# Kernel optimization log

Hardware: AMD Instinct MI355X
Metric: run time of the kernel (lower is better)

Reference implementation:

```python
import jax, jax.numpy as jnp
import numpy as np

B, N, E = 4, 10000, 640000
IN, HID, OUT, H = 128, 64, 64, 2


def _lin(key, fi, fo):
    kw, kb = jax.random.split(key)
    w = jax.random.normal(kw, (fi, fo), dtype=jnp.float32) / np.sqrt(fi)
    b = jnp.zeros((fo,), dtype=jnp.float32)
    return w, b


def setup_inputs() -> dict:
    key = jax.random.key(0)
    ks = jax.random.split(key, 12)
    x = jax.random.normal(ks[0], (B, N, IN), dtype=jnp.float32)
    edge_index = jax.random.randint(ks[1], (2, E), 0, B * N, dtype=jnp.int64)
    # layer 1: TransformerConv(IN -> HID, heads=H, concat=False)
    Wq1, bq1 = _lin(ks[2], IN, H * HID)
    Wk1, bk1 = _lin(ks[3], IN, H * HID)
    Wv1, bv1 = _lin(ks[4], IN, H * HID)
    Ws1, bs1 = _lin(ks[5], IN, HID)  # root/skip (concat=False -> out_channels)
    # layer 2: TransformerConv(HID -> OUT, heads=H, concat=False), no activation
    Wq2, bq2 = _lin(ks[6], HID, H * OUT)
    Wk2, bk2 = _lin(ks[7], HID, H * OUT)
    Wv2, bv2 = _lin(ks[8], HID, H * OUT)
    Ws2, bs2 = _lin(ks[9], HID, OUT)
    return dict(x=x, edge_index=edge_index,
                Wq1=Wq1, bq1=bq1, Wk1=Wk1, bk1=bk1, Wv1=Wv1, bv1=bv1, Ws1=Ws1, bs1=bs1,
                Wq2=Wq2, bq2=bq2, Wk2=Wk2, bk2=bk2, Wv2=Wv2, bv2=bv2, Ws2=Ws2, bs2=bs2)


def transformer_conv(x, src, dst, Wq, bq, Wk, bk, Wv, bv, Ws, bs, heads, ch):
    """PyG TransformerConv with concat=False (mean over heads) + root skip."""
    Nn = x.shape[0]
    q = (x @ Wq + bq).reshape(Nn, heads, ch)
    k = (x @ Wk + bk).reshape(Nn, heads, ch)
    v = (x @ Wv + bv).reshape(Nn, heads, ch)
    scale = 1.0 / np.sqrt(ch)
    # edge-wise attention logits: q_i . k_j / sqrt(ch)   [E, H]
    alpha = jnp.einsum('ehc,ehc->eh', q[dst], k[src]) * scale
    # numerically stable softmax over incoming edges of each destination node
    m = jax.ops.segment_max(alpha, dst, num_segments=Nn)  # [Nn, H]
    e = jnp.exp(alpha - m[dst])
    denom = jax.ops.segment_sum(e, dst, num_segments=Nn)  # [Nn, H]
    msg = jax.ops.segment_sum(e[:, :, None] * v[src], dst, num_segments=Nn)  # [Nn,H,C]
    out = msg / jnp.maximum(denom, 1e-16)[:, :, None]
    out = out.mean(axis=1)  # concat=False -> average heads
    return out + x @ Ws + bs  # root_weight skip


def reference(x, edge_index,
              Wq1, bq1, Wk1, bk1, Wv1, bv1, Ws1, bs1,
              Wq2, bq2, Wk2, bk2, Wv2, bv2, Ws2, bs2):
    bsz, n, _ = x.shape
    xf = x.reshape(bsz * n, IN)
    src, dst = edge_index[0], edge_index[1]
    h = transformer_conv(xf, src, dst, Wq1, bq1, Wk1, bk1, Wv1, bv1, Ws1, bs1, H, HID)
    h = jax.nn.leaky_relu(h, 0.1)
    o = transformer_conv(h, src, dst, Wq2, bq2, Wk2, bk2, Wv2, bv2, Ws2, bs2, H, OUT)
    return o.reshape(bsz, n, OUT)
```

## Files before the change

### kernel.cpp

```cpp
#include <hip/hip_runtime.h>
#include <math.h>

#define NN    40000
#define HEADS 2
#define CHN   64
#define NC    448
#define QSC   192

#define SCAN_BLK 256
#define NBLK ((NN + SCAN_BLK - 1) / SCAN_BLK)

__device__ __forceinline__ unsigned short f2bf(float f) {
  unsigned int u = __float_as_uint(f);
  unsigned int r = u + 0x7fffu + ((u >> 16) & 1u);
  return (unsigned short)(r >> 16);
}

__global__ void detect_k(const int* __restrict__ w, int* __restrict__ flag) {
  int lane = threadIdx.x & 63;
  int v = 0;
#pragma unroll
  for (int i = 0; i < 4; ++i) v |= w[2 * (lane + 64 * i) + 1];
#pragma unroll
  for (int o = 32; o; o >>= 1) v |= __shfl_xor(v, o);
  if (lane == 0 && blockIdx.x == 0) *flag = (v == 0) ? 1 : 0;
}

__global__ void decode_k(const int* __restrict__ w, const int* __restrict__ flag,
                         int* __restrict__ srcs, int* __restrict__ dsts,
                         int* __restrict__ deg, int E) {
  int e = blockIdx.x * blockDim.x + threadIdx.x;
  if (e >= E) return;
  int s, d;
  if (*flag) { s = w[2 * e]; d = w[2 * (E + e)]; }
  else       { s = w[e];     d = w[E + e]; }
  srcs[e] = s;
  dsts[e] = d;
  atomicAdd(&deg[d], 1);
}

__global__ void pack_all(const float* __restrict__ Wq1, const float* __restrict__ bq1,
                         const float* __restrict__ Wk1, const float* __restrict__ bk1,
                         const float* __restrict__ Wv1, const float* __restrict__ bv1,
                         const float* __restrict__ Ws1, const float* __restrict__ bs1,
                         const float* __restrict__ Wq2, const float* __restrict__ bq2,
                         const float* __restrict__ Wk2, const float* __restrict__ bk2,
                         const float* __restrict__ Wv2, const float* __restrict__ bv2,
                         const float* __restrict__ Ws2, const float* __restrict__ bs2,
                         float* __restrict__ B1, float* __restrict__ bias1,
                         float* __restrict__ B2, float* __restrict__ bias2) {
  int i = blockIdx.x * blockDim.x + threadIdx.x;
  if (i < 57344) {
    int k = i / NC, c = i % NC;
    float v;
    if (c < 128)      v = Wq1[k * 128 + c];
    else if (c < 256) v = Wk1[k * 128 + (c - 128)];
    else if (c < 384) v = Wv1[k * 128 + (c - 256)];
    else              v = Ws1[k * 64 + (c - 384)];
    B1[i] = v;
  } else if (i < 86016) {
    int j = i - 57344;
    int k = j / NC, c = j % NC;
    float v;
    if (c < 128)      v = Wq2[k * 128 + c];
    else if (c < 256) v = Wk2[k * 128 + (c - 128)];
    else if (c < 384) v = Wv2[k * 128 + (c - 256)];
    else              v = Ws2[k * 64 + (c - 384)];
    B2[j] = v;
  } else if (i < 86464) {
    int c = i - 86016;
    float v;
    if (c < 128)      v = bq1[c];
    else if (c < 256) v = bk1[c - 128];
    else if (c < 384) v = bv1[c - 256];
    else              v = bs1[c - 384];
    bias1[c] = v;
  } else if (i < 86912) {
    int c = i - 86464;
    float v;
    if (c < 128)      v = bq2[c];
    else if (c < 256) v = bk2[c - 128];
    else if (c < 384) v = bv2[c - 256];
    else              v = bs2[c - 384];
    bias2[c] = v;
  }
}

__global__ __launch_bounds__(SCAN_BLK) void bsum_k(const int* __restrict__ deg,
                                                   int* __restrict__ bsum) {
  int t = threadIdx.x;
  int i = blockIdx.x * SCAN_BLK + t;
  int v = (i < NN) ? deg[i] : 0;
#pragma unroll
  for (int o = 32; o; o >>= 1) v += __shfl_xor(v, o);
  __shared__ int ws[4];
  if ((t & 63) == 0) ws[t >> 6] = v;
  __syncthreads();
  if (t == 0) bsum[blockIdx.x] = ws[0] + ws[1] + ws[2] + ws[3];
}

__global__ __launch_bounds__(SCAN_BLK) void bscan_k(const int* __restrict__ bsum,
                                                    int* __restrict__ boff) {
  int t = threadIdx.x;
  int lane = t & 63, w = t >> 6;
  int v = (t < NBLK) ? bsum[t] : 0;
  int incl = v;
#pragma unroll
  for (int o = 1; o < 64; o <<= 1) {
    int u = __shfl_up(incl, o);
    if (lane >= o) incl += u;
  }
  __shared__ int wsum[4];
  if (lane == 63) wsum[w] = incl;
  __syncthreads();
  int woff = 0;
  for (int j = 0; j < w; ++j) woff += wsum[j];
  if (t < NBLK) boff[t] = woff + incl - v;
}

__global__ __launch_bounds__(SCAN_BLK) void rpwrite_k(const int* __restrict__ deg,
    const int* __restrict__ boff, int* __restrict__ rp, int* __restrict__ cur) {
  int t = threadIdx.x;
  int i = blockIdx.x * SCAN_BLK + t;
  int v = (i < NN) ? deg[i] : 0;
  int lane = t & 63, w = t >> 6;
  int incl = v;
#pragma unroll
  for (int o = 1; o < 64; o <<= 1) {
    int u = __shfl_up(incl, o);
    if (lane >= o) incl += u;
  }
  __shared__ int wsum[4];
  if (lane == 63) wsum[w] = incl;
  __syncthreads();
  int woff = 0;
  for (int j = 0; j < w; ++j) woff += wsum[j];
  int ex = boff[blockIdx.x] + woff + incl - v;
  if (i < NN) { rp[i] = ex; cur[i] = ex; }
  if (i == NN - 1) rp[NN] = ex + v;
}

__global__ void scatter_k(const int* __restrict__ srcs, const int* __restrict__ dsts,
                          int* __restrict__ cur, int* __restrict__ col, int E) {
  int e = blockIdx.x * blockDim.x + threadIdx.x;
  if (e < E) {
    int p = atomicAdd(&cur[dsts[e]], 1);
    col[p] = srcs[e];
  }
}

__global__ __launch_bounds__(256) void gemm_bias(const float* __restrict__ A,
    const float* __restrict__ Bm, const float* __restrict__ bias,
    float* __restrict__ QS, unsigned short* __restrict__ KVH, int M, int K) {
  __shared__ __align__(16) float As[32][68];
  __shared__ __align__(16) float Bs[32][64];
  int bm = blockIdx.y << 6, bn = blockIdx.x << 6;
  int tid = threadIdx.x;
  int tr = (tid >> 4) << 2;
  int tc = (tid & 15) << 2;
  float acc[4][4] = {};
  for (int k0 = 0; k0 < K; k0 += 32) {
#pragma unroll
    for (int t = 0; t < 2; ++t) {
      int i = tid + (t << 8);
      int m = i >> 3, k4 = (i & 7) << 2;
      const float4 va = *(const float4*)(A + (size_t)(bm + m) * K + k0 + k4);
      As[k4 + 0][m] = va.x; As[k4 + 1][m] = va.y;
      As[k4 + 2][m] = va.z; As[k4 + 3][m] = va.w;
      int kb = i >> 4, n4 = (i & 15) << 2;
      *(float4*)&Bs[kb][n4] = *(const float4*)(Bm + (size_t)(k0 + kb) * NC + bn + n4);
    }
    __syncthreads();
#pragma unroll
    for (int kk = 0; kk < 32; ++kk) {
      const float4 av = *(const float4*)&As[kk][tr];
      const float4 bv = *(const float4*)&Bs[kk][tc];
      float a[4] = {av.x, av.y, av.z, av.w};
      float b[4] = {bv.x, bv.y, bv.z, bv.w};
#pragma unroll
      for (int i2 = 0; i2 < 4; ++i2)
#pragma unroll
        for (int j = 0; j < 4; ++j) acc[i2][j] += a[i2] * b[j];
    }
    __syncthreads();
  }
  const int c0 = bn + tc;
  const float4 bb = *(const float4*)&bias[c0];
#pragma unroll
  for (int i2 = 0; i2 < 4; ++i2) {
    int row = bm + tr + i2;
    float4 o;
    o.x = acc[i2][0] + bb.x; o.y = acc[i2][1] + bb.y;
    o.z = acc[i2][2] + bb.z; o.w = acc[i2][3] + bb.w;
    if (c0 < 128) {
      *(float4*)(QS + (size_t)row * QSC + c0) = o;
    } else if (c0 < 384) {
      int isV = (c0 >= 256);
      int kc = c0 - 128 - (isV << 7);
      int hh = kc >> 6, ch = kc & 63;
      size_t off = (size_t)row * 256 + hh * 128 + (ch >> 2) * 8 + (isV << 2);
      ushort4 w4;
      w4.x = f2bf(o.x); w4.y = f2bf(o.y); w4.z = f2bf(o.z); w4.w = f2bf(o.w);
      *(ushort4*)(KVH + off) = w4;
    } else {
      *(float4*)(QS + (size_t)row * QSC + 128 + (c0 - 384)) = o;
    }
  }
}

__global__ __launch_bounds__(128) void agg_fused(const float* __restrict__ QS,
    const unsigned short* __restrict__ KVH,
    const int* __restrict__ rp, const int* __restrict__ col,
    float* __restrict__ out, int act) {
  int dst = blockIdx.x;
  int h = threadIdx.x >> 6;
  int lane = threadIdx.x & 63;
  int g = lane >> 4;
  int sl = lane & 15;
  const float scale = 0.125f;

  float4 q4 = *(const float4*)(QS + (size_t)dst * QSC + h * 64 + 4 * sl);
  q4.x *= scale; q4.y *= scale; q4.z *= scale; q4.w *= scale;
  const unsigned short* __restrict__ kvb = KVH + h * 128 + sl * 8;

  float m = -INFINITY, d = 0.f;
  float4 acc = {0.f, 0.f, 0.f, 0.f};
  int e0 = rp[dst], e1 = rp[dst + 1];

  int e = e0 + g;
  if (e < e1) {
    int sCur = col[e];
    int en = e + 4;
    int sNxt = (en < e1) ? col[en] : sCur;
    uint4 uC = *(const uint4*)(kvb + (size_t)sCur * 256);
    while (true) {
      uint4 uN = *(const uint4*)(kvb + (size_t)sNxt * 256);
      int enn = e + 8;
      int sNN = (enn < e1) ? col[enn] : sNxt;
      float k0 = __uint_as_float(uC.x << 16);
      float k1 = __uint_as_float(uC.x & 0xffff0000u);
      float k2 = __uint_as_float(uC.y << 16);
      float k3 = __uint_as_float(uC.y & 0xffff0000u);
      float p = q4.x * k0 + q4.y * k1 + q4.z * k2 + q4.w * k3;
      p += __shfl_xor(p, 1); p += __shfl_xor(p, 2);
      p += __shfl_xor(p, 4); p += __shfl_xor(p, 8);
      float mn = fmaxf(m, p);
      float corr = __expf(m - mn);
      float w = __expf(p - mn);
      float v0 = __uint_as_float(uC.z << 16);
      float v1 = __uint_as_float(uC.z & 0xffff0000u);
      float v2 = __uint_as_float(uC.w << 16);
      float v3 = __uint_as_float(uC.w & 0xffff0000u);
      d = d * corr + w;
      acc.x = acc.x * corr + w * v0;
      acc.y = acc.y * corr + w * v1;
      acc.z = acc.z * corr + w * v2;
      acc.w = acc.w * corr + w * v3;
      m = mn;
      e += 4;
      if (e >= e1) break;
      uC = uN; sNxt = sNN;
    }
  }

#pragma unroll
  for (int o = 16; o <= 32; o <<= 1) {
    float m2 = __shfl_xor(m, o);
    float d2 = __shfl_xor(d, o);
    float ax = __shfl_xor(acc.x, o), ay = __shfl_xor(acc.y, o);
    float az = __shfl_xor(acc.z, o), aw = __shfl_xor(acc.w, o);
    float mn = fmaxf(m, m2);
    float c1 = __expf(fmaxf(m - mn, -88.f));
    float c2 = __expf(fmaxf(m2 - mn, -88.f));
    d = d * c1 + d2 * c2;
    acc.x = acc.x * c1 + ax * c2;
    acc.y = acc.y * c1 + ay * c2;
    acc.z = acc.z * c1 + az * c2;
    acc.w = acc.w * c1 + aw * c2;
    m = mn;
  }
  float inv = 1.0f / fmaxf(d, 1e-16f);
  float4 r = {acc.x * inv, acc.y * inv, acc.z * inv, acc.w * inv};

  __shared__ float s1[64];
  if (h == 1 && g == 0) *(float4*)&s1[4 * sl] = r;
  __syncthreads();
  if (h == 0 && g == 0) {
    const float4 rr = *(const float4*)&s1[4 * sl];
    const float4 sk = *(const float4*)(QS + (size_t)dst * QSC + 128 + 4 * sl);
    float4 o;
    o.x = 0.5f * (r.x + rr.x) + sk.x;
    o.y = 0.5f * (r.y + rr.y) + sk.y;
    o.z = 0.5f * (r.z + rr.z) + sk.z;
    o.w = 0.5f * (r.w + rr.w) + sk.w;
    if (act) {
      o.x = o.x > 0.f ? o.x : 0.1f * o.x;
      o.y = o.y > 0.f ? o.y : 0.1f * o.y;
      o.z = o.z > 0.f ? o.z : 0.1f * o.z;
      o.w = o.w > 0.f ? o.w : 0.1f * o.w;
    }
    *(float4*)(out + (size_t)dst * CHN + 4 * sl) = o;
  }
}

extern "C" void kernel_launch(void* const* d_in, const int* in_sizes, int n_in,
                              void* d_out, int out_size, void* d_ws, size_t ws_size,
                              hipStream_t stream) {
  const float* x = (const float*)d_in[0];
  const int* ei_raw = (const int*)d_in[1];
  const float *Wq1 = (const float*)d_in[2],  *bq1 = (const float*)d_in[3],
              *Wk1 = (const float*)d_in[4],  *bk1 = (const float*)d_in[5],
              *Wv1 = (const float*)d_in[6],  *bv1 = (const float*)d_in[7],
              *Ws1 = (const float*)d_in[8],  *bs1 = (const float*)d_in[9],
              *Wq2 = (const float*)d_in[10], *bq2 = (const float*)d_in[11],
              *Wk2 = (const float*)d_in[12], *bk2 = (const float*)d_in[13],
              *Wv2 = (const float*)d_in[14], *bv2 = (const float*)d_in[15],
              *Ws2 = (const float*)d_in[16], *bs2 = (const float*)d_in[17];
  float* out = (float*)d_out;
  const int E = in_sizes[1] / 2;

  char* base = (char*)d_ws;
  size_t off = 0;
  auto take = [&](size_t bytes) {
    char* p = base + off;
    off += (bytes + 255) & ~(size_t)255;
    return p;
  };
  float* B1    = (float*)take((size_t)128 * NC * 4);
  float* bias1 = (float*)take(NC * 4);
  float* B2    = (float*)take((size_t)64 * NC * 4);
  float* bias2 = (float*)take(NC * 4);
  int*   flag  = (int*)take(256);
  int*   deg   = (int*)take((size_t)NN * 4);
  int*   rp    = (int*)take((size_t)(NN + 1) * 4);
  int*   cur   = (int*)take((size_t)(NN + 1) * 4);
  int*   bsum  = (int*)take((size_t)NBLK * 4);
  int*   boff  = (int*)take((size_t)NBLK * 4);
  int*   srcs  = (int*)take((size_t)E * 4);
  int*   dsts  = (int*)take((size_t)E * 4);
  int*   col   = (int*)take((size_t)E * 4);
  float* QS    = (float*)take((size_t)NN * QSC * 4);
  unsigned short* KVH = (unsigned short*)take((size_t)NN * 256 * 2);
  float* Hbuf  = (float*)take((size_t)NN * CHN * 4);
  (void)ws_size; (void)n_in; (void)out_size;

  hipMemsetAsync(deg, 0, (size_t)NN * 4, stream);
  pack_all<<<(86912 + 255) / 256, 256, 0, stream>>>(
      Wq1, bq1, Wk1, bk1, Wv1, bv1, Ws1, bs1,
      Wq2, bq2, Wk2, bk2, Wv2, bv2, Ws2, bs2, B1, bias1, B2, bias2);
  detect_k<<<1, 64, 0, stream>>>(ei_raw, flag);
  decode_k<<<(E + 255) / 256, 256, 0, stream>>>(ei_raw, flag, srcs, dsts, deg, E);
  bsum_k<<<NBLK, SCAN_BLK, 0, stream>>>(deg, bsum);
  bscan_k<<<1, SCAN_BLK, 0, stream>>>(bsum, boff);
  rpwrite_k<<<NBLK, SCAN_BLK, 0, stream>>>(deg, boff, rp, cur);
  scatter_k<<<(E + 255) / 256, 256, 0, stream>>>(srcs, dsts, cur, col, E);

  gemm_bias<<<dim3(NC / 64, NN / 64), 256, 0, stream>>>(x, B1, bias1, QS, KVH, NN, 128);
  agg_fused<<<NN, 128, 0, stream>>>(QS, KVH, rp, col, Hbuf, 1);

  gemm_bias<<<dim3(NC / 64, NN / 64), 256, 0, stream>>>(Hbuf, B2, bias2, QS, KVH, NN, 64);
  agg_fused<<<NN, 128, 0, stream>>>(QS, KVH, rp, col, out, 0);
}
```

Before: 362.6 us.

## Replace FP32 SIMT GEMM with split-bf16 MFMA GEMM using transposed weights

The dense projection GEMM moves from FP32 FMA loops to MFMA bf16 instructions. Each operand is split into a high and a low bf16 part, and three MFMAs per tile (hi*hi, lo*hi, hi*lo) keep accuracy close to FP32. Weights are packed transposed (column-major by output) into hi/lo bf16 buffers, and A is converted into shared memory once per block. B fragments are loaded straight from global memory, and the epilogue now writes scalars instead of float4 vectors, which may cost some store efficiency.

```diff
diff --git a/kernel.cpp b/kernel.cpp
--- a/kernel.cpp
+++ b/kernel.cpp
@@ -2,18 +2,24 @@
 #include <math.h>
 
 #define NN    40000
-#define HEADS 2
+#define QSC   192
+#define NC    448
 #define CHN   64
-#define NC    448
-#define QSC   192
 
 #define SCAN_BLK 256
 #define NBLK ((NN + SCAN_BLK - 1) / SCAN_BLK)
+#define LDA 136
+
+typedef __attribute__((ext_vector_type(8))) short bf16x8;
+typedef __attribute__((ext_vector_type(4))) float f32x4;
 
 __device__ __forceinline__ unsigned short f2bf(float f) {
   unsigned int u = __float_as_uint(f);
   unsigned int r = u + 0x7fffu + ((u >> 16) & 1u);
   return (unsigned short)(r >> 16);
+}
+__device__ __forceinline__ float bf2f(unsigned short h) {
+  return __uint_as_float((unsigned int)h << 16);
 }
 
 __global__ void detect_k(const int* __restrict__ w, int* __restrict__ flag) {
@@ -47,26 +53,31 @@
                          const float* __restrict__ Wk2, const float* __restrict__ bk2,
                          const float* __restrict__ Wv2, const float* __restrict__ bv2,
                          const float* __restrict__ Ws2, const float* __restrict__ bs2,
-                         float* __restrict__ B1, float* __restrict__ bias1,
-                         float* __restrict__ B2, float* __restrict__ bias2) {
+                         unsigned short* __restrict__ Bh1, unsigned short* __restrict__ Bl1,
+                         unsigned short* __restrict__ Bh2, unsigned short* __restrict__ Bl2,
+                         float* __restrict__ bias1, float* __restrict__ bias2) {
   int i = blockIdx.x * blockDim.x + threadIdx.x;
   if (i < 57344) {
-    int k = i / NC, c = i % NC;
+    int c = i >> 7, k = i & 127;
     float v;
     if (c < 128)      v = Wq1[k * 128 + c];
     else if (c < 256) v = Wk1[k * 128 + (c - 128)];
     else if (c < 384) v = Wv1[k * 128 + (c - 256)];
     else              v = Ws1[k * 64 + (c - 384)];
-    B1[i] = v;
+    unsigned short hi = f2bf(v);
+    Bh1[i] = hi;
+    Bl1[i] = f2bf(v - bf2f(hi));
   } else if (i < 86016) {
     int j = i - 57344;
-    int k = j / NC, c = j % NC;
+    int c = j >> 6, k = j & 63;
     float v;
     if (c < 128)      v = Wq2[k * 128 + c];
     else if (c < 256) v = Wk2[k * 128 + (c - 128)];
     else if (c < 384) v = Wv2[k * 128 + (c - 256)];
     else              v = Ws2[k * 64 + (c - 384)];
-    B2[j] = v;
+    unsigned short hi = f2bf(v);
+    Bh2[j] = hi;
+    Bl2[j] = f2bf(v - bf2f(hi));
   } else if (i < 86464) {
     int c = i - 86016;
     float v;
@@ -149,61 +160,70 @@
   }
 }
 
-__global__ __launch_bounds__(256) void gemm_bias(const float* __restrict__ A,
-    const float* __restrict__ Bm, const float* __restrict__ bias,
-    float* __restrict__ QS, unsigned short* __restrict__ KVH, int M, int K) {
-  __shared__ __align__(16) float As[32][68];
-  __shared__ __align__(16) float Bs[32][64];
+__global__ __launch_bounds__(256) void gemm_mfma(const float* __restrict__ A,
+    const unsigned short* __restrict__ Bh, const unsigned short* __restrict__ Bl,
+    const float* __restrict__ bias,
+    float* __restrict__ QS, unsigned short* __restrict__ KVH, int K) {
+  __shared__ unsigned short Ah[64 * LDA];
+  __shared__ unsigned short Al[64 * LDA];
   int bm = blockIdx.y << 6, bn = blockIdx.x << 6;
   int tid = threadIdx.x;
-  int tr = (tid >> 4) << 2;
-  int tc = (tid & 15) << 2;
-  float acc[4][4] = {};
-  for (int k0 = 0; k0 < K; k0 += 32) {
-#pragma unroll
-    for (int t = 0; t < 2; ++t) {
-      int i = tid + (t << 8);
-      int m = i >> 3, k4 = (i & 7) << 2;
-      const float4 va = *(const float4*)(A + (size_t)(bm + m) * K + k0 + k4);
-      As[k4 + 0][m] = va.x; As[k4 + 1][m] = va.y;
-      As[k4 + 2][m] = va.z; As[k4 + 3][m] = va.w;
-      int kb = i >> 4, n4 = (i & 15) << 2;
-      *(float4*)&Bs[kb][n4] = *(const float4*)(Bm + (size_t)(k0 + kb) * NC + bn + n4);
-    }
-    __syncthreads();
-#pragma unroll
-    for (int kk = 0; kk < 32; ++kk) {
-      const float4 av = *(const float4*)&As[kk][tr];
-      const float4 bv = *(const float4*)&Bs[kk][tc];
-      float a[4] = {av.x, av.y, av.z, av.w};
-      float b[4] = {bv.x, bv.y, bv.z, bv.w};
-#pragma unroll
-      for (int i2 = 0; i2 < 4; ++i2)
-#pragma unroll
-        for (int j = 0; j < 4; ++j) acc[i2][j] += a[i2] * b[j];
-    }
-    __syncthreads();
-  }
-  const int c0 = bn + tc;
-  const float4 bb = *(const float4*)&bias[c0];
-#pragma unroll
-  for (int i2 = 0; i2 < 4; ++i2) {
-    int row = bm + tr + i2;
-    float4 o;
-    o.x = acc[i2][0] + bb.x; o.y = acc[i2][1] + bb.y;
-    o.z = acc[i2][2] + bb.z; o.w = acc[i2][3] + bb.w;
-    if (c0 < 128) {
-      *(float4*)(QS + (size_t)row * QSC + c0) = o;
-    } else if (c0 < 384) {
-      int isV = (c0 >= 256);
-      int kc = c0 - 128 - (isV << 7);
-      int hh = kc >> 6, ch = kc & 63;
-      size_t off = (size_t)row * 256 + hh * 128 + (ch >> 2) * 8 + (isV << 2);
-      ushort4 w4;
-      w4.x = f2bf(o.x); w4.y = f2bf(o.y); w4.z = f2bf(o.z); w4.w = f2bf(o.w);
-      *(ushort4*)(KVH + off) = w4;
-    } else {
-      *(float4*)(QS + (size_t)row * QSC + 128 + (c0 - 384)) = o;
+  {
+    int per = K >> 2;
+    int row = tid >> 2, c0 = (tid & 3) * per;
+    const float* ga = A + (size_t)(bm + row) * K + c0;
+    unsigned short* ah = Ah + row * LDA + c0;
+    unsigned short* al = Al + row * LDA + c0;
+    for (int j = 0; j < per; j += 4) {
+      float4 v = *(const float4*)(ga + j);
+      ushort4 h, l;
+      h.x = f2bf(v.x); h.y = f2bf(v.y); h.z = f2bf(v.z); h.w = f2bf(v.w);
+      l.x = f2bf(v.x - bf2f(h.x)); l.y = f2bf(v.y - bf2f(h.y));
+      l.z = f2bf(v.z - bf2f(h.z)); l.w = f2bf(v.w - bf2f(h.w));
+      *(ushort4*)(ah + j) = h;
+      *(ushort4*)(al + j) = l;
+    }
+  }
+  __syncthreads();
+  int w = tid >> 6, l = tid & 63;
+  int lr = l & 15, lk = (l >> 4) << 3;
+  f32x4 z = {0.f, 0.f, 0.f, 0.f};
+  f32x4 acc[4] = {z, z, z, z};
+  int arow = (16 * w + lr) * LDA;
+  int ksteps = K >> 5;
+  for (int ks = 0; ks < ksteps; ++ks) {
+    int ko = (ks << 5) + lk;
+    bf16x8 a_h = *(const bf16x8*)&Ah[arow + ko];
+    bf16x8 a_l = *(const bf16x8*)&Al[arow + ko];
+#pragma unroll
+    for (int ns = 0; ns < 4; ++ns) {
+      size_t boff = (size_t)(bn + 16 * ns + lr) * K + ko;
+      bf16x8 b_h = *(const bf16x8*)(Bh + boff);
+      bf16x8 b_l = *(const bf16x8*)(Bl + boff);
+      acc[ns] = __builtin_amdgcn_mfma_f32_16x16x32_bf16(a_h, b_h, acc[ns], 0, 0, 0);
+      acc[ns] = __builtin_amdgcn_mfma_f32_16x16x32_bf16(a_l, b_h, acc[ns], 0, 0, 0);
+      acc[ns] = __builtin_amdgcn_mfma_f32_16x16x32_bf16(a_h, b_l, acc[ns], 0, 0, 0);
+    }
+  }
+  int rowb = bm + 16 * w + ((l >> 4) << 2);
+#pragma unroll
+  for (int ns = 0; ns < 4; ++ns) {
+    int c = bn + (ns << 4) + lr;
+    float bb = bias[c];
+#pragma unroll
+    for (int r = 0; r < 4; ++r) {
+      float o = acc[ns][r] + bb;
+      int row = rowb + r;
+      if (c < 128) {
+        QS[(size_t)row * QSC + c] = o;
+      } else if (c < 384) {
+        int isV = (c >= 256) ? 1 : 0;
+        int kc = c - 128 - (isV << 7);
+        int hh = kc >> 6, ch = kc & 63;
+        KVH[(size_t)row * 256 + hh * 128 + (ch >> 2) * 8 + (isV << 2) + (ch & 3)] = f2bf(o);
+      } else {
+        QS[(size_t)row * QSC + 128 + (c - 384)] = o;
+      }
     }
   }
 }
@@ -246,16 +266,16 @@
       p += __shfl_xor(p, 4); p += __shfl_xor(p, 8);
       float mn = fmaxf(m, p);
       float corr = __expf(m - mn);
-      float w = __expf(p - mn);
+      float wgt = __expf(p - mn);
       float v0 = __uint_as_float(uC.z << 16);
       float v1 = __uint_as_float(uC.z & 0xffff0000u);
       float v2 = __uint_as_float(uC.w << 16);
       float v3 = __uint_as_float(uC.w & 0xffff0000u);
-      d = d * corr + w;
-      acc.x = acc.x * corr + w * v0;
-      acc.y = acc.y * corr + w * v1;
-      acc.z = acc.z * corr + w * v2;
-      acc.w = acc.w * corr + w * v3;
+      d = d * corr + wgt;
+      acc.x = acc.x * corr + wgt * v0;
+      acc.y = acc.y * corr + wgt * v1;
+      acc.z = acc.z * corr + wgt * v2;
+      acc.w = acc.w * corr + wgt * v3;
       m = mn;
       e += 4;
       if (e >= e1) break;
@@ -326,9 +346,11 @@
     off += (bytes + 255) & ~(size_t)255;
     return p;
   };
-  float* B1    = (float*)take((size_t)128 * NC * 4);
+  unsigned short* Bh1 = (unsigned short*)take((size_t)57344 * 2);
+  unsigned short* Bl1 = (unsigned short*)take((size_t)57344 * 2);
+  unsigned short* Bh2 = (unsigned short*)take((size_t)28672 * 2);
+  unsigned short* Bl2 = (unsigned short*)take((size_t)28672 * 2);
   float* bias1 = (float*)take(NC * 4);
-  float* B2    = (float*)take((size_t)64 * NC * 4);
   float* bias2 = (float*)take(NC * 4);
   int*   flag  = (int*)take(256);
   int*   deg   = (int*)take((size_t)NN * 4);
@@ -347,7 +369,8 @@
   hipMemsetAsync(deg, 0, (size_t)NN * 4, stream);
   pack_all<<<(86912 + 255) / 256, 256, 0, stream>>>(
       Wq1, bq1, Wk1, bk1, Wv1, bv1, Ws1, bs1,
-      Wq2, bq2, Wk2, bk2, Wv2, bv2, Ws2, bs2, B1, bias1, B2, bias2);
+      Wq2, bq2, Wk2, bk2, Wv2, bv2, Ws2, bs2,
+      Bh1, Bl1, Bh2, Bl2, bias1, bias2);
   detect_k<<<1, 64, 0, stream>>>(ei_raw, flag);
   decode_k<<<(E + 255) / 256, 256, 0, stream>>>(ei_raw, flag, srcs, dsts, deg, E);
   bsum_k<<<NBLK, SCAN_BLK, 0, stream>>>(deg, bsum);
@@ -355,9 +378,9 @@
   rpwrite_k<<<NBLK, SCAN_BLK, 0, stream>>>(deg, boff, rp, cur);
   scatter_k<<<(E + 255) / 256, 256, 0, stream>>>(srcs, dsts, cur, col, E);
 
-  gemm_bias<<<dim3(NC / 64, NN / 64), 256, 0, stream>>>(x, B1, bias1, QS, KVH, NN, 128);
+  gemm_mfma<<<dim3(7, NN / 64), 256, 0, stream>>>(x, Bh1, Bl1, bias1, QS, KVH, 128);
   agg_fused<<<NN, 128, 0, stream>>>(QS, KVH, rp, col, Hbuf, 1);
 
-  gemm_bias<<<dim3(NC / 64, NN / 64), 256, 0, stream>>>(Hbuf, B2, bias2, QS, KVH, NN, 64);
+  gemm_mfma<<<dim3(7, NN / 64), 256, 0, stream>>>(Hbuf, Bh2, Bl2, bias2, QS, KVH, 64);
   agg_fused<<<NN, 128, 0, stream>>>(QS, KVH, rp, col, out, 0);
 }
```

Result: slower. 430.7 us (+18.8%).
